# Kernel tuning notes

Measured on AMD Instinct MI355X. Metric: run time of the kernel, lower is better.

The kernel has to match this reference:

```python
import jax, jax.numpy as jnp
import numpy as np

N_LAYERS = 8
DILATIONS = [1, 2, 1, 2, 1, 2, 1, 2]
K_HOPS = 3
BN = 13248   # batch(64) * n_nodes(207), merged as in the torch module
L = 13       # 12 history steps + 1; shrinks by sum(dilations)=12 across layers
E = 211968   # BN * avg_degree(16)


def _conv1d(x, w, b, dil):
    # x: (BN, Cin, L), w: (Cout, Cin, 2) kernel-2 dilated conv, VALID (causal shrink)
    y = jax.lax.conv_general_dilated(x, w, (1,), 'VALID', rhs_dilation=(dil,),
                                     dimension_numbers=('NCH', 'OIH', 'NCH'))
    return y + b[None, :, None]


def setup_inputs() -> dict:
    key = jax.random.key(0)
    ks = jax.random.split(key, 20)
    s = 0.1  # keep activations in a sane range
    return {
        'x': jax.random.normal(ks[0], (BN, L, 2), jnp.float32),
        'edge_src': jax.random.randint(ks[1], (E,), 0, BN),
        'edge_dst': jax.random.randint(ks[2], (E,), 0, BN),
        'edge_w': jax.random.uniform(ks[3], (E,), jnp.float32),
        'init_w': s * jax.random.normal(ks[4], (2, 32), jnp.float32),
        'init_b': s * jax.random.normal(ks[5], (32,), jnp.float32),
        'filt_w': s * jax.random.normal(ks[6], (8, 32, 32, 2), jnp.float32),
        'filt_b': s * jax.random.normal(ks[7], (8, 32), jnp.float32),
        'gate_w': s * jax.random.normal(ks[8], (8, 32, 32, 2), jnp.float32),
        'gate_b': s * jax.random.normal(ks[9], (8, 32), jnp.float32),
        'gcn_w': s * jax.random.normal(ks[10], (8, 6, 32, 32), jnp.float32),
        'gcn_b': s * jax.random.normal(ks[11], (8, 32), jnp.float32),
        'skip_w': s * jax.random.normal(ks[12], (8, 256, 32), jnp.float32),
        'skip_b': s * jax.random.normal(ks[13], (8, 256), jnp.float32),
        'out0_w': s * jax.random.normal(ks[14], (256, 512), jnp.float32),
        'out0_b': s * jax.random.normal(ks[15], (512,), jnp.float32),
        'out1_w': s * jax.random.normal(ks[16], (512, 12), jnp.float32),
        'out1_b': s * jax.random.normal(ks[17], (12,), jnp.float32),
    }


def reference(x, edge_src, edge_dst, edge_w, init_w, init_b,
              filt_w, filt_b, gate_w, gate_b, gcn_w, gcn_b,
              skip_w, skip_b, out0_w, out0_b, out1_w, out1_b):
    # init linear: (BN, L, 2) -> (BN, L, 32) -> (BN, 32, L)
    h = (x @ init_w + init_b).transpose(0, 2, 1)
    # per-hop edge weights: elementwise powers of the transition weights
    # (faithful to repo's dense_to_sparse(transition ** k)); bck = transposed edges
    adjs = [(edge_src, edge_dst, edge_w ** k) for k in range(1, K_HOPS + 1)] + \
           [(edge_dst, edge_src, edge_w ** k) for k in range(1, K_HOPS + 1)]
    skip = None
    for l in range(N_LAYERS):
        d = DILATIONS[l]
        res = h
        # Gated TCN: tanh(filter) * sigmoid(gate), seq shrinks by d
        t = jnp.tanh(_conv1d(h, filt_w[l], filt_b[l], d)) * \
            jax.nn.sigmoid(_conv1d(h, gate_w[l], gate_b[l], d))
        # Diffusion conv: sum over 6 adjacency types of A_w (x W_a)
        xt = t.transpose(0, 2, 1)  # (BN, L', 32)
        g = jnp.zeros_like(xt)
        for a, (src, dst, w) in enumerate(adjs):
            msg = (xt @ gcn_w[l, a])[src] * w[:, None, None]  # (E, L', 32)
            g = g + jax.ops.segment_sum(msg, dst, num_segments=BN)
        h = g.transpose(0, 2, 1) + gcn_b[l][None, :, None]  # (BN, 32, L')
        # residual connection (align shrunk sequence)
        h = h + res[:, :, -h.shape[-1]:]
        # skip conv (1x1) on last timestep, accumulated
        sc = h[:, :, -1] @ skip_w[l].T + skip_b[l]  # (BN, 256)
        skip = sc if skip is None else skip + sc
    out = jax.nn.relu(skip)
    out = jax.nn.relu(out @ out0_w + out0_b)
    return out @ out1_w + out1_b  # (BN, 12)
```

## Files before the change

kernel.cpp:

```cpp
#include <hip/hip_runtime.h>
#include <hip/hip_fp16.h>

#define BN 13248
#define NE 211968
#define ZSTRIDE 200

typedef __attribute__((ext_vector_type(8))) short bf16x8;
typedef __attribute__((ext_vector_type(8))) _Float16 f16x8;
typedef __attribute__((ext_vector_type(4))) float f32x4;

__device__ __forceinline__ f32x4 mfma16b(bf16x8 a, bf16x8 b, f32x4 c) {
  return __builtin_amdgcn_mfma_f32_16x16x32_bf16(a, b, c, 0, 0, 0);
}
__device__ __forceinline__ f32x4 mfma16h(f16x8 a, f16x8 b, f32x4 c) {
  return __builtin_amdgcn_mfma_f32_16x16x32_f16(a, b, c, 0, 0, 0);
}

__device__ __forceinline__ unsigned short to_bf16(float v) {
  unsigned bits = __float_as_uint(v);
  return (unsigned short)((bits + 0x7FFFu + ((bits >> 16) & 1u)) >> 16);
}
__device__ __forceinline__ unsigned short to_f16(float v) {
  union { __half h; unsigned short s; } u; u.h = __float2half(v); return u.s;
}
__device__ __forceinline__ unsigned h2u(__half2 h) {
  union { __half2 h; unsigned u; } v; v.h = h; return v.u;
}
__device__ __forceinline__ __half2 u2h(unsigned u) {
  union { unsigned u; __half2 h; } v; v.u = u; return v.h;
}

__device__ __forceinline__ float fast_tanh(float x) {
  float e2 = __expf(2.f * x);
  return 1.f - 2.f / (e2 + 1.f);
}
__device__ __forceinline__ float fast_sig(float x) {
  return 1.f / (1.f + __expf(-x));
}

__global__ void k_count(const int* __restrict__ src, const int* __restrict__ dst,
                        int* __restrict__ cur_f, int* __restrict__ cur_b) {
  int e = blockIdx.x * 256 + threadIdx.x;
  if (e < NE) {
    atomicAdd(&cur_f[dst[e]], 1);
    atomicAdd(&cur_b[src[e]], 1);
  }
}

__global__ void k_scan(int* __restrict__ cur_f, int* __restrict__ row_f,
                       int* __restrict__ cur_b, int* __restrict__ row_b) {
  __shared__ int sdata[1024];
  int tid = threadIdx.x;
  for (int which = 0; which < 2; ++which) {
    int* cnt = which ? cur_b : cur_f;
    int* row = which ? row_b : row_f;
    int base = tid * 13;
    int vals[13];
    int tot = 0;
    for (int k = 0; k < 13; ++k) {
      int idx = base + k;
      int v = (idx < BN) ? cnt[idx] : 0;
      vals[k] = v; tot += v;
    }
    sdata[tid] = tot;
    __syncthreads();
    for (int off = 1; off < 1024; off <<= 1) {
      int add = (tid >= off) ? sdata[tid - off] : 0;
      __syncthreads();
      sdata[tid] += add;
      __syncthreads();
    }
    int running = sdata[tid] - tot;
    for (int k = 0; k < 13; ++k) {
      int idx = base + k;
      if (idx < BN) { row[idx] = running; cnt[idx] = running; running += vals[k]; }
    }
    if (tid == 1023) row[BN] = sdata[1023];
    __syncthreads();
  }
}

__global__ void k_fill(const int* __restrict__ src, const int* __restrict__ dst,
                       const float* __restrict__ w,
                       int* __restrict__ cur_f, int4* __restrict__ ce_f,
                       int* __restrict__ cur_b, int4* __restrict__ ce_b) {
  int e = blockIdx.x * 256 + threadIdx.x;
  if (e < NE) {
    int s = src[e], t = dst[e];
    float wv = w[e];
    float w2 = wv * wv, w3 = w2 * wv;
    int u1 = (int)h2u(__float2half2_rn(wv));
    int u2 = (int)h2u(__float2half2_rn(w2));
    int u3 = (int)h2u(__float2half2_rn(w3));
    int p = atomicAdd(&cur_f[t], 1); ce_f[p] = make_int4(s, u1, u2, u3);
    int q = atomicAdd(&cur_b[s], 1); ce_b[q] = make_int4(t, u1, u2, u3);
  }
}

__global__ void k_init(const float* __restrict__ x, const float* __restrict__ iw,
                       const float* __restrict__ ib, float* __restrict__ h) {
  int idx = blockIdx.x * 256 + threadIdx.x;
  if (idx >= BN * 13 * 32) return;
  int c = idx & 31;
  int r = idx >> 5;
  int n = r % BN;
  int tau = r / BN;
  float x0 = x[(n * 13 + tau) * 2 + 0];
  float x1 = x[(n * 13 + tau) * 2 + 1];
  h[idx] = fmaf(x0, iw[c], fmaf(x1, iw[32 + c], ib[c]));
}

__global__ void k_pack(const float* __restrict__ skip_w, const float* __restrict__ skip_b,
                       const float* __restrict__ w0, const float* __restrict__ w1,
                       const float* __restrict__ gcn_w,
                       const float* __restrict__ filt_w, const float* __restrict__ gate_w,
                       unsigned short* __restrict__ SWb, unsigned short* __restrict__ W0T,
                       unsigned short* __restrict__ W1T, float* __restrict__ bsum,
                       unsigned short* __restrict__ Gg16, uint2* __restrict__ WQ2) {
  int id = blockIdx.x * 256 + threadIdx.x;
  if (id < 65536) {
    int j = id >> 8, k = id & 255;
    SWb[id] = to_bf16(skip_w[((k >> 5) * 256 + j) * 32 + (k & 31)]);
  }
  if (id < 131072) {
    int jo = id >> 8, k = id & 255;
    W0T[id] = to_bf16(w0[k * 512 + jo]);
  }
  if (id < 8192) {
    int n = id >> 9, k = id & 511;
    W1T[id] = (n < 12) ? to_bf16(w1[k * 12 + n]) : (unsigned short)0;
  }
  if (id < 256) {
    float s = 0.f;
    for (int l = 0; l < 8; ++l) s += skip_b[l * 256 + id];
    bsum[id] = s;
  }
  if (id < 49152) {
    int l = id / 6144, rem = id % 6144;
    int co = rem / 192, k = rem % 192;
    int a = k >> 5, ci = k & 31;
    Gg16[id] = to_f16(gcn_w[((l * 6 + a) * 32 + ci) * 32 + co]);
  }
  if (id < 7168) {
    int l = id / 1024 + 1, rem = id % 1024;
    int ci = rem >> 5, co = rem & 31;
    const float* fw = filt_w + l * 2048;
    const float* gw = gate_w + l * 2048;
    __half2 a, b;
    a.x = __float2half(fw[(co * 32 + ci) * 2 + 0]); a.y = __float2half(gw[(co * 32 + ci) * 2 + 0]);
    b.x = __float2half(fw[(co * 32 + ci) * 2 + 1]); b.y = __float2half(gw[(co * 32 + ci) * 2 + 1]);
    WQ2[id] = make_uint2(h2u(a), h2u(b));
  }
}

template<int LIN, int D, int TPAD>
__global__ __launch_bounds__(256) void k_tcn(const float* __restrict__ h_in, unsigned short* __restrict__ t_out,
    const float* __restrict__ fw, const float* __restrict__ fb,
    const float* __restrict__ gw, const float* __restrict__ gb) {
  constexpr int LOUT = LIN - D;
  __shared__ __align__(16) float wq[32 * 32 * 4];
  __shared__ float hl[8][LIN * 32];
  int tid = threadIdx.x;
  for (int f = tid; f < 4096; f += 256) {
    int e = f & 3, co = (f >> 2) & 31, ci = f >> 7;
    const float* srcw = (e < 2) ? fw : gw;
    wq[f] = srcw[(co * 32 + ci) * 2 + (e & 1)];
  }
  int n0 = blockIdx.x * 8;
  for (int i = tid; i < 8 * LIN * 32; i += 256) {
    int c = i & 31, r = i >> 5;
    int nl = r / LIN, tau = r % LIN;
    hl[nl][tau * 32 + c] = h_in[(tau * BN + n0 + nl) * 32 + c];
  }
  __syncthreads();
  int nl = tid >> 5, co = tid & 31;
  int n = n0 + nl;
  float accf[LOUT], accg[LOUT];
  float fbv = fb[co], gbv = gb[co];
#pragma unroll
  for (int j = 0; j < LOUT; ++j) { accf[j] = fbv; accg[j] = gbv; }
#pragma unroll
  for (int ci = 0; ci < 32; ++ci) {
    float4 wv = *(const float4*)&wq[(ci * 32 + co) * 4];
    float xr[LIN];
#pragma unroll
    for (int t = 0; t < LIN; ++t) xr[t] = hl[nl][t * 32 + ci];
#pragma unroll
    for (int j = 0; j < LOUT; ++j) {
      accf[j] = fmaf(xr[j], wv.x, accf[j]);
      accf[j] = fmaf(xr[j + D], wv.y, accf[j]);
      accg[j] = fmaf(xr[j], wv.z, accg[j]);
      accg[j] = fmaf(xr[j + D], wv.w, accg[j]);
    }
  }
#pragma unroll
  for (int j = 0; j < TPAD; ++j) {
    unsigned short v = 0;
    if (j < LOUT) v = to_f16(fast_tanh(accf[j < LOUT ? j : 0]) * fast_sig(accg[j < LOUT ? j : 0]));
    t_out[(n * TPAD + j) * 32 + co] = v;
  }
}

template<int TPAD, int NT>
__device__ __forceinline__ void edge_fma(const int4& c, const uint2 (&u)[NT], __half2* A) {
  __half2 wh0 = u2h((unsigned)c.y), wh1 = u2h((unsigned)c.z), wh2 = u2h((unsigned)c.w);
#pragma unroll
  for (int j = 0; j < NT; ++j) {
    __half2 v0 = u2h(u[j].x), v1 = u2h(u[j].y);
    A[(0 * NT + j) * 2 + 0] = __hfma2(wh0, v0, A[(0 * NT + j) * 2 + 0]);
    A[(0 * NT + j) * 2 + 1] = __hfma2(wh0, v1, A[(0 * NT + j) * 2 + 1]);
    A[(1 * NT + j) * 2 + 0] = __hfma2(wh1, v0, A[(1 * NT + j) * 2 + 0]);
    A[(1 * NT + j) * 2 + 1] = __hfma2(wh1, v1, A[(1 * NT + j) * 2 + 1]);
    A[(2 * NT + j) * 2 + 0] = __hfma2(wh2, v0, A[(2 * NT + j) * 2 + 0]);
    A[(2 * NT + j) * 2 + 1] = __hfma2(wh2, v1, A[(2 * NT + j) * 2 + 1]);
  }
}

template<int TPAD, int NT>
__device__ __forceinline__ void gather_dir(const unsigned short* __restrict__ t_in,
    int e0, int e1, const int4* __restrict__ ce, int rowoff0, __half2* A) {
  constexpr int EB = 4;
  int e = e0;
  if (e + EB <= e1) {
    int4 c[EB];
#pragma unroll
    for (int k = 0; k < EB; ++k) c[k] = ce[e + k];
    while (true) {
      uint2 u[EB][NT];
#pragma unroll
      for (int k = 0; k < EB; ++k) {
        const unsigned short* p = t_in + c[k].x * (TPAD * 32) + rowoff0;
#pragma unroll
        for (int j = 0; j < NT; ++j) u[k][j] = *(const uint2*)(p + j * 32);
      }
      int en = e + EB;
      bool more = (en + EB <= e1);
      int pb = more ? en : e;
      int4 cn[EB];
#pragma unroll
      for (int k = 0; k < EB; ++k) cn[k] = ce[pb + k];
#pragma unroll
      for (int k = 0; k < EB; ++k) edge_fma<TPAD, NT>(c[k], u[k], A);
#pragma unroll
      for (int k = 0; k < EB; ++k) c[k] = cn[k];
      e = en;
      if (!more) break;
    }
  }
  for (; e < e1; ++e) {
    int4 c = ce[e];
    uint2 u[NT];
    const unsigned short* p = t_in + c.x * (TPAD * 32) + rowoff0;
#pragma unroll
    for (int j = 0; j < NT; ++j) u[j] = *(const uint2*)(p + j * 32);
    edge_fma<TPAD, NT>(c, u, A);
  }
}

template<int LOUT, int D, int TPAD, int D2, int TPAD2, bool LAST>
__global__ __launch_bounds__(128, 4) void k_fused(
    const unsigned short* __restrict__ t_in,
    const float* __restrict__ h_in, float* __restrict__ h_out,
    float* __restrict__ lastcol, unsigned short* __restrict__ t_next,
    const int* __restrict__ row_f, const int4* __restrict__ ce_f,
    const int* __restrict__ row_b, const int4* __restrict__ ce_b,
    const unsigned short* __restrict__ Wg,
    const float* __restrict__ bias,
    const uint2* __restrict__ WQn,
    const float* __restrict__ fbn, const float* __restrict__ gbn) {
  constexpr int NT = TPAD / 4;
  constexpr int LIN2 = LOUT;
  constexpr int LOUT2 = LAST ? 1 : (LOUT - D2);
  constexpr int ZBYTES = 4 * TPAD * ZSTRIDE * 2;
  constexpr int PBYTES = LAST ? 0 : (8192 + 4 * LIN2 * 33 * 4);
  constexpr int SBYTES = (ZBYTES > PBYTES) ? ZBYTES : PBYTES;
  __shared__ __align__(16) char smem[SBYTES];
  unsigned short* Zl = (unsigned short*)smem;
  uint2* wq2s = (uint2*)smem;
  float* hbuf = (float*)(smem + 8192);
  int tid = threadIdx.x;
  int nl = tid >> 5, lane32 = tid & 31;
  int tl = lane32 >> 3;
  int c4 = (lane32 & 7) << 2;
  int n0 = blockIdx.x * 4;
  int n = n0 + nl;
  int rowoff0 = (tl * NT) * 32 + c4;
  int ef0 = row_f[n], ef1 = row_f[n + 1];
  int eb0 = row_b[n], eb1 = row_b[n + 1];
  __half2 acc[6 * NT * 2];
  __half2 zero = __float2half2_rn(0.f);
#pragma unroll
  for (int i = 0; i < 6 * NT * 2; ++i) acc[i] = zero;
  gather_dir<TPAD, NT>(t_in, ef0, ef1, ce_f, rowoff0, acc);
  gather_dir<TPAD, NT>(t_in, eb0, eb1, ce_b, rowoff0, acc + 3 * NT * 2);
#pragma unroll
  for (int j = 0; j < NT; ++j) {
    int m = nl * TPAD + tl * NT + j;
#pragma unroll
    for (int a = 0; a < 6; ++a) {
      uint2 v = make_uint2(h2u(acc[(a * NT + j) * 2 + 0]), h2u(acc[(a * NT + j) * 2 + 1]));
      *(uint2*)(&Zl[m * ZSTRIDE + a * 32 + c4]) = v;
    }
  }
  __syncthreads();
  int wave = tid >> 6, lane = tid & 63;
  int m16 = lane & 15, q = lane >> 4;
  f32x4 dacc[NT];
#pragma unroll
  for (int i = 0; i < NT; ++i) {
    int u = wave * NT + i;
    int mt = u >> 1, nt = u & 1;
    dacc[i] = (f32x4){0.f, 0.f, 0.f, 0.f};
#pragma unroll
    for (int ks = 0; ks < 6; ++ks) {
      f16x8 av = *(const f16x8*)(&Zl[(mt * 16 + m16) * ZSTRIDE + ks * 32 + q * 8]);
      f16x8 bv = *(const f16x8*)((const _Float16*)Wg + (nt * 16 + m16) * 192 + ks * 32 + q * 8);
      dacc[i] = mfma16h(av, bv, dacc[i]);
    }
  }
  __syncthreads();
  if (!LAST) {
    for (int i = tid; i < 1024; i += 128) wq2s[i] = WQn[i];
  }
#pragma unroll
  for (int i = 0; i < NT; ++i) {
    int u = wave * NT + i;
    int mt = u >> 1, nt = u & 1;
    int co = nt * 16 + m16;
    float bco = bias[co];
#pragma unroll
    for (int r = 0; r < 4; ++r) {
      int mm = mt * 16 + q * 4 + r;
      int node = n0 + mm / TPAD;
      int tau = mm % TPAD;
      if (tau < LOUT) {
        float rres = h_in[((tau + D) * BN + node) * 32 + co];
        float o = dacc[i][r] + bco + rres;
        h_out[(tau * BN + node) * 32 + co] = o;
        if (!LAST) hbuf[(mm / TPAD) * (LIN2 * 33) + tau * 33 + co] = o;
        if (tau == LOUT - 1) lastcol[node * 32 + co] = o;
      }
    }
  }
  if (!LAST) {
    __syncthreads();
    int co = lane32;
    float accf[LOUT2], accg[LOUT2];
    float fbv = fbn[co], gbv = gbn[co];
#pragma unroll
    for (int j = 0; j < LOUT2; ++j) { accf[j] = fbv; accg[j] = gbv; }
    const float* hb = &hbuf[nl * (LIN2 * 33)];
#pragma unroll
    for (int ci = 0; ci < 32; ++ci) {
      uint2 wp = wq2s[ci * 32 + co];
      __half2 wa = u2h(wp.x), wb = u2h(wp.y);
      float wf0 = __low2float(wa), wg0 = __high2float(wa);
      float wf1 = __low2float(wb), wg1 = __high2float(wb);
      float xr[LIN2];
#pragma unroll
      for (int t = 0; t < LIN2; ++t) xr[t] = hb[t * 33 + ci];
#pragma unroll
      for (int j = 0; j < LOUT2; ++j) {
        accf[j] = fmaf(xr[j], wf0, accf[j]);
        accf[j] = fmaf(xr[j + D2], wf1, accf[j]);
        accg[j] = fmaf(xr[j], wg0, accg[j]);
        accg[j] = fmaf(xr[j + D2], wg1, accg[j]);
      }
    }
#pragma unroll
    for (int j = 0; j < TPAD2; ++j) {
      unsigned short v = 0;
      if (j < LOUT2) v = to_f16(fast_tanh(accf[j < LOUT2 ? j : 0]) * fast_sig(accg[j < LOUT2 ? j : 0]));
      t_next[(n * TPAD2 + j) * 32 + co] = v;
    }
  }
}

__device__ __forceinline__ bf16x8 ldsA(const unsigned short* buf, int stride, int row, int ks, int q) {
  int unit = ks * 4 + q;
  int addr = row * stride + ((unit ^ (row & 7)) << 3);
  return *(const bf16x8*)(buf + addr);
}

__global__ __launch_bounds__(256) void k_final(const float* __restrict__ lastcol,
    const unsigned short* __restrict__ SWb, const unsigned short* __restrict__ W0T,
    const unsigned short* __restrict__ W1T, const float* __restrict__ bsum,
    const float* __restrict__ b0, const float* __restrict__ b1,
    float* __restrict__ out) {
  __shared__ __align__(16) unsigned short Z[32 * 256];
  __shared__ __align__(16) unsigned short H[32 * 512];
  int tid = threadIdx.x;
  int wave = tid >> 6, lane = tid & 63;
  int m16 = lane & 15, q = lane >> 4;
  int n0 = blockIdx.x * 32;
#pragma unroll
  for (int it = 0; it < 32; ++it) {
    int id = it * 256 + tid;
    int m = id >> 8, k = id & 255;
    float v = lastcol[((k >> 5) * BN + n0 + m) * 32 + (k & 31)];
    Z[m * 256 + (((k >> 3) ^ (m & 7)) << 3) + (k & 7)] = to_bf16(v);
  }
  __syncthreads();
  f32x4 acc1[2][4];
#pragma unroll
  for (int mt = 0; mt < 2; ++mt)
#pragma unroll
    for (int i = 0; i < 4; ++i) acc1[mt][i] = (f32x4){0.f, 0.f, 0.f, 0.f};
#pragma unroll
  for (int ks = 0; ks < 8; ++ks) {
    bf16x8 a0 = ldsA(Z, 256, m16, ks, q);
    bf16x8 a1 = ldsA(Z, 256, 16 + m16, ks, q);
#pragma unroll
    for (int i = 0; i < 4; ++i) {
      int j = (wave * 4 + i) * 16 + m16;
      bf16x8 b = *(const bf16x8*)(SWb + j * 256 + ks * 32 + q * 8);
      acc1[0][i] = mfma16b(a0, b, acc1[0][i]);
      acc1[1][i] = mfma16b(a1, b, acc1[1][i]);
    }
  }
  __syncthreads();
#pragma unroll
  for (int i = 0; i < 4; ++i) {
    int j = (wave * 4 + i) * 16 + m16;
    float bs = bsum[j];
#pragma unroll
    for (int mt = 0; mt < 2; ++mt)
#pragma unroll
      for (int r = 0; r < 4; ++r) {
        int row = mt * 16 + q * 4 + r;
        float v = fmaxf(acc1[mt][i][r] + bs, 0.f);
        Z[row * 256 + (((j >> 3) ^ (row & 7)) << 3) + (j & 7)] = to_bf16(v);
      }
  }
  __syncthreads();
  f32x4 acc2[2][8];
#pragma unroll
  for (int mt = 0; mt < 2; ++mt)
#pragma unroll
    for (int i = 0; i < 8; ++i) acc2[mt][i] = (f32x4){0.f, 0.f, 0.f, 0.f};
#pragma unroll
  for (int ks = 0; ks < 8; ++ks) {
    bf16x8 a0 = ldsA(Z, 256, m16, ks, q);
    bf16x8 a1 = ldsA(Z, 256, 16 + m16, ks, q);
#pragma unroll
    for (int i = 0; i < 8; ++i) {
      int jo = (wave * 8 + i) * 16 + m16;
      bf16x8 b = *(const bf16x8*)(W0T + jo * 256 + ks * 32 + q * 8);
      acc2[0][i] = mfma16b(a0, b, acc2[0][i]);
      acc2[1][i] = mfma16b(a1, b, acc2[1][i]);
    }
  }
#pragma unroll
  for (int i = 0; i < 8; ++i) {
    int jo = (wave * 8 + i) * 16 + m16;
    float b0v = b0[jo];
#pragma unroll
    for (int mt = 0; mt < 2; ++mt)
#pragma unroll
      for (int r = 0; r < 4; ++r) {
        int row = mt * 16 + q * 4 + r;
        float v = fmaxf(acc2[mt][i][r] + b0v, 0.f);
        H[row * 512 + (((jo >> 3) ^ (row & 7)) << 3) + (jo & 7)] = to_bf16(v);
      }
  }
  __syncthreads();
  if (wave < 2) {
    f32x4 acc3 = (f32x4){0.f, 0.f, 0.f, 0.f};
#pragma unroll
    for (int ks = 0; ks < 16; ++ks) {
      bf16x8 a = ldsA(H, 512, wave * 16 + m16, ks, q);
      bf16x8 b = *(const bf16x8*)(W1T + m16 * 512 + ks * 32 + q * 8);
      acc3 = mfma16b(a, b, acc3);
    }
    if (m16 < 12) {
      float bv = b1[m16];
#pragma unroll
      for (int r = 0; r < 4; ++r)
        out[(n0 + wave * 16 + q * 4 + r) * 12 + m16] = acc3[r] + bv;
    }
  }
}

extern "C" void kernel_launch(void* const* d_in, const int* in_sizes, int n_in,
                              void* d_out, int out_size, void* d_ws, size_t ws_size,
                              hipStream_t stream) {
  const float* x      = (const float*)d_in[0];
  const int*   esrc   = (const int*)d_in[1];
  const int*   edst   = (const int*)d_in[2];
  const float* ew     = (const float*)d_in[3];
  const float* init_w = (const float*)d_in[4];
  const float* init_b = (const float*)d_in[5];
  const float* filt_w = (const float*)d_in[6];
  const float* filt_b = (const float*)d_in[7];
  const float* gate_w = (const float*)d_in[8];
  const float* gate_b = (const float*)d_in[9];
  const float* gcn_w  = (const float*)d_in[10];
  const float* gcn_b  = (const float*)d_in[11];
  const float* skip_w = (const float*)d_in[12];
  const float* skip_b = (const float*)d_in[13];
  const float* w0     = (const float*)d_in[14];
  const float* b0     = (const float*)d_in[15];
  const float* w1     = (const float*)d_in[16];
  const float* b1     = (const float*)d_in[17];
  float* out = (float*)d_out;

  float* base = (float*)d_ws;
  float* hA      = base;
  float* hB      = hA + 13 * BN * 32;
  unsigned short* tA = (unsigned short*)(hB + 13 * BN * 32);
  unsigned short* tB = tA + 12 * BN * 32;
  float* lastcol = (float*)(tB + 12 * BN * 32);
  int* row_f = (int*)(lastcol + 8 * BN * 32);
  int* row_b = row_f + (BN + 2);
  int* cur_f = row_b + (BN + 2);
  int* cur_b = cur_f + BN;
  int4* ce_f = (int4*)(cur_b + BN + 2);
  int4* ce_b = ce_f + NE;
  unsigned short* SWb  = (unsigned short*)(ce_b + NE);
  unsigned short* W0T  = SWb + 65536;
  unsigned short* W1T  = W0T + 131072;
  unsigned short* Gg16 = W1T + 8192;
  uint2* WQ2   = (uint2*)(Gg16 + 49152);
  float* bsumv = (float*)(WQ2 + 7168);

  hipMemsetAsync(cur_f, 0, 2 * BN * sizeof(int), stream);
  const int egrid = (NE + 255) / 256;
  k_count<<<egrid, 256, 0, stream>>>(esrc, edst, cur_f, cur_b);
  k_scan<<<1, 1024, 0, stream>>>(cur_f, row_f, cur_b, row_b);
  k_fill<<<egrid, 256, 0, stream>>>(esrc, edst, ew, cur_f, ce_f, cur_b, ce_b);
  k_init<<<(BN * 13 * 32 + 255) / 256, 256, 0, stream>>>(x, init_w, init_b, hA);
  k_pack<<<512, 256, 0, stream>>>(skip_w, skip_b, w0, w1, gcn_w, filt_w, gate_w,
                                  SWb, W0T, W1T, bsumv, Gg16, WQ2);

  k_tcn<13, 1, 12><<<BN / 8, 256, 0, stream>>>(hA, tA, filt_w, filt_b, gate_w, gate_b);

#define FUSED(l, LOUTv, Dv, TPv, D2v, TP2v, LASTv, tin, tout, hin, hout) \
  k_fused<LOUTv, Dv, TPv, D2v, TP2v, LASTv><<<BN / 4, 128, 0, stream>>>( \
      tin, hin, hout, lastcol + l * BN * 32, tout, row_f, ce_f, row_b, ce_b, \
      Gg16 + l * 6144, gcn_b + l * 32, WQ2 + l * 1024, filt_b + (l + 1) * 32, gate_b + (l + 1) * 32);

  FUSED(0, 12, 1, 12, 2, 12, false, tA, tB, hA, hB)
  FUSED(1, 10, 2, 12, 1, 12, false, tB, tA, hB, hA)
  FUSED(2,  9, 1, 12, 2,  8, false, tA, tB, hA, hB)
  FUSED(3,  7, 2,  8, 1,  8, false, tB, tA, hB, hA)
  FUSED(4,  6, 1,  8, 2,  4, false, tA, tB, hA, hB)
  FUSED(5,  4, 2,  4, 1,  4, false, tB, tA, hB, hA)
  FUSED(6,  3, 1,  4, 2,  4, false, tA, tB, hA, hB)
#undef FUSED
  k_fused<1, 2, 4, 2, 4, true><<<BN / 4, 128, 0, stream>>>(
      tB, hB, hA, lastcol + 7 * BN * 32, tA, row_f, ce_f, row_b, ce_b,
      Gg16 + 7 * 6144, gcn_b + 7 * 32, WQ2, filt_b, gate_b);

  k_final<<<BN / 32, 256, 0, stream>>>(lastcol, SWb, W0T, W1T, bsumv, b0, b1, out);
}
```

Measured before the change: 666.2 us.

## Compute next-layer gated TCN conv with f16 MFMA instead of scalar FMAs

The fused diffusion kernel's epilogue, which computes the next layer's filter and gate dilated convolutions, now stages the layer output in shared memory as f16 and runs 16x16x32 f16 MFMAs. Packed weights (filter and gate, both taps concatenated along K) are read straight from global memory instead of being copied to LDS. This replaces per-lane scalar fp32 FMA loops over 32 input channels and shrinks the shared-memory footprint. The edge-gather loop also drops its software prefetch of the next edge batch and becomes a simpler loop. It costs fp16 rounding of the conv inputs, and the gather may lose some latency hiding.

```diff
diff --git a/kernel.cpp b/kernel.cpp
--- a/kernel.cpp
+++ b/kernel.cpp
@@ -4,6 +4,8 @@
 #define BN 13248
 #define NE 211968
 #define ZSTRIDE 200
+#define HSTRIDE 40
+#define HNODE 480
 
 typedef __attribute__((ext_vector_type(8))) short bf16x8;
 typedef __attribute__((ext_vector_type(8))) _Float16 f16x8;
@@ -116,7 +118,7 @@
                        const float* __restrict__ filt_w, const float* __restrict__ gate_w,
                        unsigned short* __restrict__ SWb, unsigned short* __restrict__ W0T,
                        unsigned short* __restrict__ W1T, float* __restrict__ bsum,
-                       unsigned short* __restrict__ Gg16, uint2* __restrict__ WQ2) {
+                       unsigned short* __restrict__ Gg16, unsigned short* __restrict__ WTC) {
   int id = blockIdx.x * 256 + threadIdx.x;
   if (id < 65536) {
     int j = id >> 8, k = id & 255;
@@ -141,15 +143,12 @@
     int a = k >> 5, ci = k & 31;
     Gg16[id] = to_f16(gcn_w[((l * 6 + a) * 32 + ci) * 32 + co]);
   }
-  if (id < 7168) {
-    int l = id / 1024 + 1, rem = id % 1024;
-    int ci = rem >> 5, co = rem & 31;
-    const float* fw = filt_w + l * 2048;
-    const float* gw = gate_w + l * 2048;
-    __half2 a, b;
-    a.x = __float2half(fw[(co * 32 + ci) * 2 + 0]); a.y = __float2half(gw[(co * 32 + ci) * 2 + 0]);
-    b.x = __float2half(fw[(co * 32 + ci) * 2 + 1]); b.y = __float2half(gw[(co * 32 + ci) * 2 + 1]);
-    WQ2[id] = make_uint2(h2u(a), h2u(b));
+  if (id < 32768) {
+    int l = id >> 12, rem = id & 4095;
+    int g = rem >> 11, co = (rem >> 6) & 31, k = rem & 63;
+    const float* srcw = (g ? gate_w : filt_w) + l * 2048;
+    float v = (k < 32) ? srcw[(co * 32 + k) * 2 + 0] : srcw[(co * 32 + (k - 32)) * 2 + 1];
+    WTC[id] = to_f16(v);
   }
 }
 
@@ -221,31 +220,19 @@
     int e0, int e1, const int4* __restrict__ ce, int rowoff0, __half2* A) {
   constexpr int EB = 4;
   int e = e0;
-  if (e + EB <= e1) {
+  for (; e + EB <= e1; e += EB) {
     int4 c[EB];
+    uint2 u[EB][NT];
 #pragma unroll
     for (int k = 0; k < EB; ++k) c[k] = ce[e + k];
-    while (true) {
-      uint2 u[EB][NT];
-#pragma unroll
-      for (int k = 0; k < EB; ++k) {
-        const unsigned short* p = t_in + c[k].x * (TPAD * 32) + rowoff0;
-#pragma unroll
-        for (int j = 0; j < NT; ++j) u[k][j] = *(const uint2*)(p + j * 32);
-      }
-      int en = e + EB;
-      bool more = (en + EB <= e1);
-      int pb = more ? en : e;
-      int4 cn[EB];
-#pragma unroll
-      for (int k = 0; k < EB; ++k) cn[k] = ce[pb + k];
-#pragma unroll
-      for (int k = 0; k < EB; ++k) edge_fma<TPAD, NT>(c[k], u[k], A);
-#pragma unroll
-      for (int k = 0; k < EB; ++k) c[k] = cn[k];
-      e = en;
-      if (!more) break;
-    }
+#pragma unroll
+    for (int k = 0; k < EB; ++k) {
+      const unsigned short* p = t_in + c[k].x * (TPAD * 32) + rowoff0;
+#pragma unroll
+      for (int j = 0; j < NT; ++j) u[k][j] = *(const uint2*)(p + j * 32);
+    }
+#pragma unroll
+    for (int k = 0; k < EB; ++k) edge_fma<TPAD, NT>(c[k], u[k], A);
   }
   for (; e < e1; ++e) {
     int4 c = ce[e];
@@ -266,18 +253,14 @@
     const int* __restrict__ row_b, const int4* __restrict__ ce_b,
     const unsigned short* __restrict__ Wg,
     const float* __restrict__ bias,
-    const uint2* __restrict__ WQn,
+    const unsigned short* __restrict__ Wtc,
     const float* __restrict__ fbn, const float* __restrict__ gbn) {
   constexpr int NT = TPAD / 4;
-  constexpr int LIN2 = LOUT;
   constexpr int LOUT2 = LAST ? 1 : (LOUT - D2);
-  constexpr int ZBYTES = 4 * TPAD * ZSTRIDE * 2;
-  constexpr int PBYTES = LAST ? 0 : (8192 + 4 * LIN2 * 33 * 4);
-  constexpr int SBYTES = (ZBYTES > PBYTES) ? ZBYTES : PBYTES;
+  constexpr int SBYTES = 4 * TPAD * ZSTRIDE * 2;
   __shared__ __align__(16) char smem[SBYTES];
   unsigned short* Zl = (unsigned short*)smem;
-  uint2* wq2s = (uint2*)smem;
-  float* hbuf = (float*)(smem + 8192);
+  unsigned short* hb16 = (unsigned short*)smem;
   int tid = threadIdx.x;
   int nl = tid >> 5, lane32 = tid & 31;
   int tl = lane32 >> 3;
@@ -319,9 +302,6 @@
     }
   }
   __syncthreads();
-  if (!LAST) {
-    for (int i = tid; i < 1024; i += 128) wq2s[i] = WQn[i];
-  }
 #pragma unroll
   for (int i = 0; i < NT; ++i) {
     int u = wave * NT + i;
@@ -331,47 +311,45 @@
 #pragma unroll
     for (int r = 0; r < 4; ++r) {
       int mm = mt * 16 + q * 4 + r;
-      int node = n0 + mm / TPAD;
+      int node = mm / TPAD;
       int tau = mm % TPAD;
       if (tau < LOUT) {
-        float rres = h_in[((tau + D) * BN + node) * 32 + co];
+        float rres = h_in[((tau + D) * BN + n0 + node) * 32 + co];
         float o = dacc[i][r] + bco + rres;
-        h_out[(tau * BN + node) * 32 + co] = o;
-        if (!LAST) hbuf[(mm / TPAD) * (LIN2 * 33) + tau * 33 + co] = o;
-        if (tau == LOUT - 1) lastcol[node * 32 + co] = o;
+        h_out[(tau * BN + n0 + node) * 32 + co] = o;
+        if (!LAST) hb16[node * HNODE + tau * HSTRIDE + co] = to_f16(o);
+        if (tau == LOUT - 1) lastcol[(n0 + node) * 32 + co] = o;
       }
     }
   }
   if (!LAST) {
     __syncthreads();
-    int co = lane32;
-    float accf[LOUT2], accg[LOUT2];
-    float fbv = fbn[co], gbv = gbn[co];
-#pragma unroll
-    for (int j = 0; j < LOUT2; ++j) { accf[j] = fbv; accg[j] = gbv; }
-    const float* hb = &hbuf[nl * (LIN2 * 33)];
-#pragma unroll
-    for (int ci = 0; ci < 32; ++ci) {
-      uint2 wp = wq2s[ci * 32 + co];
-      __half2 wa = u2h(wp.x), wb = u2h(wp.y);
-      float wf0 = __low2float(wa), wg0 = __high2float(wa);
-      float wf1 = __low2float(wb), wg1 = __high2float(wb);
-      float xr[LIN2];
-#pragma unroll
-      for (int t = 0; t < LIN2; ++t) xr[t] = hb[t * 33 + ci];
-#pragma unroll
-      for (int j = 0; j < LOUT2; ++j) {
-        accf[j] = fmaf(xr[j], wf0, accf[j]);
-        accf[j] = fmaf(xr[j + D2], wf1, accf[j]);
-        accg[j] = fmaf(xr[j], wg0, accg[j]);
-        accg[j] = fmaf(xr[j + D2], wg1, accg[j]);
+#pragma unroll
+    for (int i = 0; i < 4; ++i) {
+      int u = wave * 4 + i;
+      int node = u >> 1, ntc = u & 1;
+      int co = ntc * 16 + m16;
+      f32x4 df = (f32x4){0.f, 0.f, 0.f, 0.f};
+      f32x4 dg = (f32x4){0.f, 0.f, 0.f, 0.f};
+#pragma unroll
+      for (int s = 0; s < 2; ++s) {
+        f16x8 av = *(const f16x8*)(&hb16[node * HNODE + (m16 + s * D2) * HSTRIDE + q * 8]);
+        f16x8 bvf = *(const f16x8*)((const _Float16*)Wtc + (0 * 32 + co) * 64 + s * 32 + q * 8);
+        f16x8 bvg = *(const f16x8*)((const _Float16*)Wtc + (1 * 32 + co) * 64 + s * 32 + q * 8);
+        df = mfma16h(av, bvf, df);
+        dg = mfma16h(av, bvg, dg);
       }
-    }
-#pragma unroll
-    for (int j = 0; j < TPAD2; ++j) {
-      unsigned short v = 0;
-      if (j < LOUT2) v = to_f16(fast_tanh(accf[j < LOUT2 ? j : 0]) * fast_sig(accg[j < LOUT2 ? j : 0]));
-      t_next[(n * TPAD2 + j) * 32 + co] = v;
+      float fbv = fbn[co], gbv = gbn[co];
+#pragma unroll
+      for (int r = 0; r < 4; ++r) {
+        int j = q * 4 + r;
+        if (j < TPAD2) {
+          unsigned short v = 0;
+          if (j < LOUT2)
+            v = to_f16(fast_tanh(df[r] + fbv) * fast_sig(dg[r] + gbv));
+          t_next[((n0 + node) * TPAD2 + j) * 32 + co] = v;
+        }
+      }
     }
   }
 }
@@ -520,8 +498,8 @@
   unsigned short* W0T  = SWb + 65536;
   unsigned short* W1T  = W0T + 131072;
   unsigned short* Gg16 = W1T + 8192;
-  uint2* WQ2   = (uint2*)(Gg16 + 49152);
-  float* bsumv = (float*)(WQ2 + 7168);
+  unsigned short* WTC  = Gg16 + 49152;
+  float* bsumv = (float*)(WTC + 32768);
 
   hipMemsetAsync(cur_f, 0, 2 * BN * sizeof(int), stream);
   const int egrid = (NE + 255) / 256;
@@ -530,14 +508,15 @@
   k_fill<<<egrid, 256, 0, stream>>>(esrc, edst, ew, cur_f, ce_f, cur_b, ce_b);
   k_init<<<(BN * 13 * 32 + 255) / 256, 256, 0, stream>>>(x, init_w, init_b, hA);
   k_pack<<<512, 256, 0, stream>>>(skip_w, skip_b, w0, w1, gcn_w, filt_w, gate_w,
-                                  SWb, W0T, W1T, bsumv, Gg16, WQ2);
+                                  SWb, W0T, W1T, bsumv, Gg16, WTC);
 
   k_tcn<13, 1, 12><<<BN / 8, 256, 0, stream>>>(hA, tA, filt_w, filt_b, gate_w, gate_b);
 
 #define FUSED(l, LOUTv, Dv, TPv, D2v, TP2v, LASTv, tin, tout, hin, hout) \
   k_fused<LOUTv, Dv, TPv, D2v, TP2v, LASTv><<<BN / 4, 128, 0, stream>>>( \
       tin, hin, hout, lastcol + l * BN * 32, tout, row_f, ce_f, row_b, ce_b, \
-      Gg16 + l * 6144, gcn_b + l * 32, WQ2 + l * 1024, filt_b + (l + 1) * 32, gate_b + (l + 1) * 32);
+      Gg16 + l * 6144, gcn_b + l * 32, WTC + (l + 1) * 4096, \
+      filt_b + (l + 1) * 32, gate_b + (l + 1) * 32);
 
   FUSED(0, 12, 1, 12, 2, 12, false, tA, tB, hA, hB)
   FUSED(1, 10, 2, 12, 1, 12, false, tB, tA, hB, hA)
@@ -549,7 +528,7 @@
 #undef FUSED
   k_fused<1, 2, 4, 2, 4, true><<<BN / 4, 128, 0, stream>>>(
       tB, hB, hA, lastcol + 7 * BN * 32, tA, row_f, ce_f, row_b, ce_b,
-      Gg16 + 7 * 6144, gcn_b + 7 * 32, WQ2, filt_b, gate_b);
+      Gg16 + 7 * 6144, gcn_b + 7 * 32, WTC, filt_b, gate_b);
 
   k_final<<<BN / 32, 256, 0, stream>>>(lastcol, SWb, W0T, W1T, bsumv, b0, b1, out);
 }
```

Measured after the change: 684.3 us. 2.7% more time.
